# Optimization experiments

Hardware: AMD Instinct MI355X
Metric: run time of the kernel (lower is better)

Reference implementation:

```python
import jax, jax.numpy as jnp
import numpy as np

K = 100000      # tag vocab size
D_CLIP = 512    # Chinese-CLIP text dim
D_HID = 1024    # ProjectionHead hidden
D_OUT = 256     # proj_dim
B, P = 1024, 50
EPS = 1e-12


def setup_inputs() -> dict:
    key = jax.random.key(0)
    k_tab, k_ids, k_w1, k_b1, k_w2, k_b2 = jax.random.split(key, 6)
    # Frozen, L2-normalised base embeddings [K, 512]
    tab = jax.random.normal(k_tab, (K, D_CLIP), dtype=jnp.float32)
    tab = tab / jnp.maximum(jnp.linalg.norm(tab, axis=-1, keepdims=True), EPS)
    # tag ids in [-1, K): -1 marks padding rows
    tag_ids = jax.random.randint(k_ids, (B, P), -1, K, dtype=jnp.int64)
    # ProjectionHead params: Linear(512,1024) -> GELU -> Linear(1024,256)
    w1 = jax.random.normal(k_w1, (D_CLIP, D_HID), dtype=jnp.float32) * (1.0 / np.sqrt(D_CLIP))
    b1 = jnp.zeros((D_HID,), dtype=jnp.float32)
    w2 = jax.random.normal(k_w2, (D_HID, D_OUT), dtype=jnp.float32) * (1.0 / np.sqrt(D_HID))
    b2 = jnp.zeros((D_OUT,), dtype=jnp.float32)
    return {"tag_base_embs": tab, "w1": w1, "b1": b1, "w2": w2, "b2": b2,
            "tag_ids": tag_ids}


def reference(tag_base_embs, w1, b1, w2, b2, tag_ids):
    pad_mask = tag_ids < 0                       # [B, P]
    clamped = jnp.maximum(tag_ids, 0)
    flat = tag_base_embs[clamped.reshape(-1)]    # [B*P, 512] gather
    h = jax.nn.gelu(flat @ w1 + b1)              # [B*P, 1024]
    y = h @ w2 + b2                              # [B*P, 256]
    y = y / jnp.maximum(jnp.linalg.norm(y, axis=-1, keepdims=True), EPS)
    y = y.reshape(tag_ids.shape[0], tag_ids.shape[1], -1)  # [B, P, 256]
    return jnp.where(pad_mask[..., None], 0.0, y)
```

## Files before the change

kernel.cpp:

```cpp
#include <hip/hip_runtime.h>
#include <hip/hip_bf16.h>
#include <cstdint>


typedef __bf16 bf16;
typedef bf16  bf16x8 __attribute__((ext_vector_type(8)));
typedef bf16  bf16x4 __attribute__((ext_vector_type(4)));
typedef float f32x4  __attribute__((ext_vector_type(4)));

#define D_IN    512
#define D_HID   1024
#define D_OUT   256
#define MT      64
#define CHUNK   256
#define NCH     4
#define NKS1    16
#define NKS2C   8
#define THREADS 512

#define OFF_A    0
#define OFF_H    65536
#define OFF_NS   (65536 + 65536)
#define OFF_RID  (65536 + 65536 + 2048)
#define LDS_TOTAL (65536 + 65536 + 2048 + 256)

#define W1F_ELEMS (64 * 16 * 64 * 8)

__device__ __forceinline__ float gelu_tanh(float x) {
  float u = 0.7978845608028654f * (x + 0.044715f * x * x * x);
  return x * __builtin_amdgcn_rcpf(1.0f + __expf(-2.0f * u));
}

__global__ void prep_weights(const float* __restrict__ w1, const float* __restrict__ w2,
                             bf16* __restrict__ w1f, bf16* __restrict__ w2f) {
  const int t = blockIdx.x * blockDim.x + threadIdx.x;
  if (t < 65536) {
    const int l  = t & 63;
    const int ks = (t >> 6) & 15;
    const int ct = t >> 10;
    const int col   = ct * 16 + (l & 15);
    const int kbase = ks * 32 + (l >> 4) * 8;
    bf16x8 o;
#pragma unroll
    for (int j = 0; j < 8; ++j) o[j] = (bf16)w1[(size_t)(kbase + j) * D_HID + col];
    *(bf16x8*)(w1f + (size_t)t * 8) = o;
  } else if (t < 65536 + 32768) {
    const int t2 = t - 65536;
    const int l   = t2 & 63;
    const int ks2 = (t2 >> 6) & 31;
    const int ct2 = t2 >> 11;
    const int col   = ct2 * 16 + (l & 15);
    const int kbase = ks2 * 32 + (l >> 4) * 8;
    bf16x8 o;
#pragma unroll
    for (int j = 0; j < 8; ++j) o[j] = (bf16)w2[(size_t)(kbase + j) * D_OUT + col];
    *(bf16x8*)(w2f + (size_t)t2 * 8) = o;
  }
}

__global__ __launch_bounds__(THREADS, 2)
void tagproj_fused(const float* __restrict__ tab, const int* __restrict__ ids,
                   const bf16* __restrict__ w1f, const bf16* __restrict__ w2f,
                   const float* __restrict__ b1, const float* __restrict__ b2,
                   float* __restrict__ out) {
  extern __shared__ __align__(16) char lds[];
  bf16*  As  = (bf16*)(lds + OFF_A);
  bf16*  Hb  = (bf16*)(lds + OFF_H);
  float* Ns  = (float*)(lds + OFF_NS);
  int*   Rid = (int*)(lds + OFF_RID);

  const int tid = threadIdx.x;
  const int w   = tid >> 6;
  const int l   = tid & 63;
  const int lg  = l >> 4;
  const int lc  = l & 15;
  const int m0  = blockIdx.x * MT;

  {
    const int row = tid >> 3;
    const int q   = tid & 7;
    const int id  = ids[m0 + row];
    if (q == 0) Rid[row] = id;
    const float* src = tab + (size_t)(id < 0 ? 0 : id) * D_IN;
#pragma unroll
    for (int i = 0; i < 16; ++i) {
      const int c4 = i * 32 + q * 4;
      const float4 v = *(const float4*)(src + c4);
      bf16x4 b;
      b[0] = (bf16)v.x; b[1] = (bf16)v.y; b[2] = (bf16)v.z; b[3] = (bf16)v.w;
      *(bf16x4*)&As[row * 512 + (c4 ^ ((row & 15) << 3))] = b;
    }
  }
  __syncthreads();

  f32x4 acc2[4][2];
#pragma unroll
  for (int rt = 0; rt < 4; ++rt)
#pragma unroll
    for (int t = 0; t < 2; ++t) acc2[rt][t] = (f32x4){0.f, 0.f, 0.f, 0.f};

  for (int c = 0; c < NCH; ++c) {
    bf16* Hs = Hb + (c & 1) * (MT * CHUNK);

    f32x4 acc1[4][2];
#pragma unroll
    for (int rt = 0; rt < 4; ++rt)
#pragma unroll
      for (int t = 0; t < 2; ++t) acc1[rt][t] = (f32x4){0.f, 0.f, 0.f, 0.f};

    const bf16* w1p = w1f + (((size_t)(c * 16 + w * 2) * 16) * 64 + l) * 8;

    bf16x8 wr1[4][2];
#pragma unroll
    for (int pf = 0; pf < 2; ++pf)
#pragma unroll
      for (int t = 0; t < 2; ++t)
        wr1[pf][t] = *(const bf16x8*)(w1p + (size_t)t * 8192 + (size_t)pf * 512);

#pragma unroll
    for (int ks = 0; ks < NKS1; ++ks) {
      if (ks + 2 < NKS1) {
#pragma unroll
        for (int t = 0; t < 2; ++t)
          wr1[(ks + 2) & 3][t] =
              *(const bf16x8*)(w1p + (size_t)t * 8192 + (size_t)(ks + 2) * 512);
      }
      bf16x8 af[4];
#pragma unroll
      for (int rt = 0; rt < 4; ++rt) {
        const int e = ks * 32 + lg * 8;
        af[rt] = *(const bf16x8*)&As[(rt * 16 + lc) * 512 + (e ^ (lc << 3))];
      }
#pragma unroll
      for (int t = 0; t < 2; ++t)
#pragma unroll
        for (int rt = 0; rt < 4; ++rt)
          acc1[rt][t] = __builtin_amdgcn_mfma_f32_16x16x32_bf16(
              af[rt], wr1[ks & 3][t], acc1[rt][t], 0, 0, 0);
    }

#pragma unroll
    for (int t = 0; t < 2; ++t) {
      const int pos    = w * 2 + t;
      const float bias = b1[c * CHUNK + pos * 16 + lc];
#pragma unroll
      for (int rt = 0; rt < 4; ++rt) {
#pragma unroll
        for (int r = 0; r < 4; ++r) {
          const float x  = acc1[rt][t][r] + bias;
          const float hx = gelu_tanh(x);
          const int row  = rt * 16 + lg * 4 + r;
          const int e    = pos * 16 + lc;
          Hs[row * 256 + (e ^ ((row & 15) << 3))] = (bf16)hx;
        }
      }
    }
    __syncthreads();

    const bf16* w2p = w2f + (((size_t)(w * 2) * 32 + c * 8) * 64 + l) * 8;

    bf16x8 wr2[4][2];
#pragma unroll
    for (int pf = 0; pf < 2; ++pf)
#pragma unroll
      for (int t = 0; t < 2; ++t)
        wr2[pf][t] = *(const bf16x8*)(w2p + (size_t)t * 16384 + (size_t)pf * 512);

#pragma unroll
    for (int s2 = 0; s2 < NKS2C; ++s2) {
      if (s2 + 2 < NKS2C) {
#pragma unroll
        for (int t = 0; t < 2; ++t)
          wr2[(s2 + 2) & 3][t] =
              *(const bf16x8*)(w2p + (size_t)t * 16384 + (size_t)(s2 + 2) * 512);
      }
      bf16x8 hf[4];
#pragma unroll
      for (int rt = 0; rt < 4; ++rt) {
        const int e = s2 * 32 + lg * 8;
        hf[rt] = *(const bf16x8*)&Hs[(rt * 16 + lc) * 256 + (e ^ (lc << 3))];
      }
#pragma unroll
      for (int t = 0; t < 2; ++t)
#pragma unroll
        for (int rt = 0; rt < 4; ++rt)
          acc2[rt][t] = __builtin_amdgcn_mfma_f32_16x16x32_bf16(
              hf[rt], wr2[s2 & 3][t], acc2[rt][t], 0, 0, 0);
    }
  }

  float yv[4][2][4];
  float ssq[4][4];
#pragma unroll
  for (int rt = 0; rt < 4; ++rt)
#pragma unroll
    for (int r = 0; r < 4; ++r) ssq[rt][r] = 0.f;

#pragma unroll
  for (int t = 0; t < 2; ++t) {
    const float bias = b2[(w * 2 + t) * 16 + lc];
#pragma unroll
    for (int rt = 0; rt < 4; ++rt)
#pragma unroll
      for (int r = 0; r < 4; ++r) {
        const float v = acc2[rt][t][r] + bias;
        yv[rt][t][r] = v;
        ssq[rt][r] += v * v;
      }
  }
#pragma unroll
  for (int rt = 0; rt < 4; ++rt)
#pragma unroll
    for (int r = 0; r < 4; ++r) {
      float s = ssq[rt][r];
      s += __shfl_xor(s, 1);
      s += __shfl_xor(s, 2);
      s += __shfl_xor(s, 4);
      s += __shfl_xor(s, 8);
      ssq[rt][r] = s;
    }
  if (lc == 0) {
#pragma unroll
    for (int rt = 0; rt < 4; ++rt)
#pragma unroll
      for (int r = 0; r < 4; ++r)
        Ns[(rt * 16 + lg * 4 + r) * 8 + w] = ssq[rt][r];
  }
  __syncthreads();

#pragma unroll
  for (int rt = 0; rt < 4; ++rt)
#pragma unroll
    for (int r = 0; r < 4; ++r) {
      const int row = rt * 16 + lg * 4 + r;
      float ss = 0.f;
#pragma unroll
      for (int ww = 0; ww < 8; ++ww) ss += Ns[row * 8 + ww];
      const float scale = (Rid[row] < 0) ? 0.f : (1.f / fmaxf(sqrtf(ss), 1e-12f));
#pragma unroll
      for (int t = 0; t < 2; ++t)
        out[(size_t)(m0 + row) * D_OUT + (w * 2 + t) * 16 + lc] = yv[rt][t][r] * scale;
    }
}

extern "C" void kernel_launch(void* const* d_in, const int* in_sizes, int n_in,
                              void* d_out, int out_size, void* d_ws, size_t ws_size,
                              hipStream_t stream) {
  const float* tab = (const float*)d_in[0];
  const float* w1  = (const float*)d_in[1];
  const float* b1  = (const float*)d_in[2];
  const float* w2  = (const float*)d_in[3];
  const float* b2  = (const float*)d_in[4];
  const int*   ids = (const int*)d_in[5];
  float* out = (float*)d_out;

  bf16* w1f = (bf16*)d_ws;
  bf16* w2f = w1f + W1F_ELEMS;

  hipLaunchKernelGGL(prep_weights, dim3(384), dim3(256), 0, stream, w1, w2, w1f, w2f);

  (void)hipFuncSetAttribute(reinterpret_cast<const void*>(tagproj_fused),
                            hipFuncAttributeMaxDynamicSharedMemorySize, LDS_TOTAL);
  hipLaunchKernelGGL(tagproj_fused, dim3(51200 / MT), dim3(THREADS), LDS_TOTAL, stream,
                     tab, ids, w1f, w2f, b1, b2, out);
}
```

Before: 183.3 us.

## Rebalance rows per block with 32-row tiles and exact single-wave grid

Each block now owns 100 consecutive rows, processed as three 32-row tiles plus a 4-row tail tile. The launch is 512 blocks. Halving the tile size halves LDS use, so two blocks can be resident per CU and the whole grid fits in one wave. This removes the partial final wave of the old 800-block, 64-row launch. In exchange each weight fragment loaded from L2 feeds half as many MFMA rows, which doubles weight traffic, and the tail tile wastes MFMA work on padded rows.

```diff
diff --git a/kernel.cpp b/kernel.cpp
--- a/kernel.cpp
+++ b/kernel.cpp
@@ -11,18 +11,20 @@
 #define D_IN    512
 #define D_HID   1024
 #define D_OUT   256
-#define MT      64
+#define MT      32
+#define RPB     100
 #define CHUNK   256
 #define NCH     4
 #define NKS1    16
 #define NKS2C   8
 #define THREADS 512
+#define NROWS   51200
 
 #define OFF_A    0
-#define OFF_H    65536
-#define OFF_NS   (65536 + 65536)
-#define OFF_RID  (65536 + 65536 + 2048)
-#define LDS_TOTAL (65536 + 65536 + 2048 + 256)
+#define OFF_H    32768
+#define OFF_NS   (32768 + 32768)
+#define OFF_RID  (32768 + 32768 + 1024)
+#define LDS_TOTAL (32768 + 32768 + 1024 + 128)
 
 #define W1F_ELEMS (64 * 16 * 64 * 8)
 
@@ -58,7 +60,187 @@
   }
 }
 
-__global__ __launch_bounds__(THREADS, 2)
+template<int RT, int RV>
+__device__ __forceinline__ void process_tile(
+    const float* __restrict__ tab, const int* __restrict__ ids,
+    const bf16* __restrict__ w1f, const bf16* __restrict__ w2f,
+    const float* __restrict__ b1, const float* __restrict__ b2,
+    float* __restrict__ out,
+    bf16* As, bf16* Hb, float* Ns, int* Rid,
+    int row0, int tid, int w, int l, int lg, int lc) {
+
+  __syncthreads();
+
+  {
+    const int row = tid >> 4;
+    const int q   = tid & 15;
+    int id = -1;
+    if (RV == MT || row < RV) id = ids[row0 + row];
+    if (q == 0) Rid[row] = id;
+    const float* src = tab + (size_t)(id < 0 ? 0 : id) * D_IN;
+#pragma unroll
+    for (int i = 0; i < 8; ++i) {
+      const int c4 = i * 64 + q * 4;
+      const float4 v = *(const float4*)(src + c4);
+      bf16x4 b;
+      b[0] = (bf16)v.x; b[1] = (bf16)v.y; b[2] = (bf16)v.z; b[3] = (bf16)v.w;
+      *(bf16x4*)&As[row * 512 + (c4 ^ ((row & 15) << 3))] = b;
+    }
+  }
+  __syncthreads();
+
+  f32x4 acc2[RT][2];
+#pragma unroll
+  for (int rt = 0; rt < RT; ++rt)
+#pragma unroll
+    for (int t = 0; t < 2; ++t) acc2[rt][t] = (f32x4){0.f, 0.f, 0.f, 0.f};
+
+  for (int c = 0; c < NCH; ++c) {
+    bf16* Hs = Hb + (c & 1) * (MT * CHUNK);
+
+    f32x4 acc1[RT][2];
+#pragma unroll
+    for (int rt = 0; rt < RT; ++rt)
+#pragma unroll
+      for (int t = 0; t < 2; ++t) acc1[rt][t] = (f32x4){0.f, 0.f, 0.f, 0.f};
+
+    const bf16* w1p = w1f + (((size_t)(c * 16 + w * 2) * 16) * 64 + l) * 8;
+    bf16x8 wr1[4][2];
+#pragma unroll
+    for (int pf = 0; pf < 2; ++pf)
+#pragma unroll
+      for (int t = 0; t < 2; ++t)
+        wr1[pf][t] = *(const bf16x8*)(w1p + (size_t)t * 8192 + (size_t)pf * 512);
+
+#pragma unroll
+    for (int ks = 0; ks < NKS1; ++ks) {
+      if (ks + 2 < NKS1) {
+#pragma unroll
+        for (int t = 0; t < 2; ++t)
+          wr1[(ks + 2) & 3][t] =
+              *(const bf16x8*)(w1p + (size_t)t * 8192 + (size_t)(ks + 2) * 512);
+      }
+      bf16x8 af[RT];
+#pragma unroll
+      for (int rt = 0; rt < RT; ++rt) {
+        const int e = ks * 32 + lg * 8;
+        af[rt] = *(const bf16x8*)&As[(rt * 16 + lc) * 512 + (e ^ (lc << 3))];
+      }
+#pragma unroll
+      for (int t = 0; t < 2; ++t)
+#pragma unroll
+        for (int rt = 0; rt < RT; ++rt)
+          acc1[rt][t] = __builtin_amdgcn_mfma_f32_16x16x32_bf16(
+              af[rt], wr1[ks & 3][t], acc1[rt][t], 0, 0, 0);
+    }
+
+#pragma unroll
+    for (int t = 0; t < 2; ++t) {
+      const int pos    = w * 2 + t;
+      const float bias = b1[c * CHUNK + pos * 16 + lc];
+#pragma unroll
+      for (int rt = 0; rt < RT; ++rt) {
+#pragma unroll
+        for (int r = 0; r < 4; ++r) {
+          const float x  = acc1[rt][t][r] + bias;
+          const float hx = gelu_tanh(x);
+          const int row  = rt * 16 + lg * 4 + r;
+          const int e    = pos * 16 + lc;
+          Hs[row * 256 + (e ^ ((row & 15) << 3))] = (bf16)hx;
+        }
+      }
+    }
+    __syncthreads();
+
+    const bf16* w2p = w2f + (((size_t)(w * 2) * 32 + c * 8) * 64 + l) * 8;
+    bf16x8 wr2[4][2];
+#pragma unroll
+    for (int pf = 0; pf < 2; ++pf)
+#pragma unroll
+      for (int t = 0; t < 2; ++t)
+        wr2[pf][t] = *(const bf16x8*)(w2p + (size_t)t * 16384 + (size_t)pf * 512);
+
+#pragma unroll
+    for (int s2 = 0; s2 < NKS2C; ++s2) {
+      if (s2 + 2 < NKS2C) {
+#pragma unroll
+        for (int t = 0; t < 2; ++t)
+          wr2[(s2 + 2) & 3][t] =
+              *(const bf16x8*)(w2p + (size_t)t * 16384 + (size_t)(s2 + 2) * 512);
+      }
+      bf16x8 hf[RT];
+#pragma unroll
+      for (int rt = 0; rt < RT; ++rt) {
+        const int e = s2 * 32 + lg * 8;
+        hf[rt] = *(const bf16x8*)&Hs[(rt * 16 + lc) * 256 + (e ^ (lc << 3))];
+      }
+#pragma unroll
+      for (int t = 0; t < 2; ++t)
+#pragma unroll
+        for (int rt = 0; rt < RT; ++rt)
+          acc2[rt][t] = __builtin_amdgcn_mfma_f32_16x16x32_bf16(
+              hf[rt], wr2[s2 & 3][t], acc2[rt][t], 0, 0, 0);
+    }
+  }
+
+  float yv[RT][2][4];
+  float ssq[RT][4];
+#pragma unroll
+  for (int rt = 0; rt < RT; ++rt)
+#pragma unroll
+    for (int r = 0; r < 4; ++r) ssq[rt][r] = 0.f;
+
+#pragma unroll
+  for (int t = 0; t < 2; ++t) {
+    const float bias = b2[(w * 2 + t) * 16 + lc];
+#pragma unroll
+    for (int rt = 0; rt < RT; ++rt)
+#pragma unroll
+      for (int r = 0; r < 4; ++r) {
+        const float v = acc2[rt][t][r] + bias;
+        yv[rt][t][r] = v;
+        ssq[rt][r] += v * v;
+      }
+  }
+#pragma unroll
+  for (int rt = 0; rt < RT; ++rt)
+#pragma unroll
+    for (int r = 0; r < 4; ++r) {
+      float s = ssq[rt][r];
+      s += __shfl_xor(s, 1);
+      s += __shfl_xor(s, 2);
+      s += __shfl_xor(s, 4);
+      s += __shfl_xor(s, 8);
+      ssq[rt][r] = s;
+    }
+  if (lc == 0) {
+#pragma unroll
+    for (int rt = 0; rt < RT; ++rt)
+#pragma unroll
+      for (int r = 0; r < 4; ++r)
+        Ns[(rt * 16 + lg * 4 + r) * 8 + w] = ssq[rt][r];
+  }
+  __syncthreads();
+
+#pragma unroll
+  for (int rt = 0; rt < RT; ++rt)
+#pragma unroll
+    for (int r = 0; r < 4; ++r) {
+      const int row = rt * 16 + lg * 4 + r;
+      if (RV == MT || row < RV) {
+        float ss = 0.f;
+#pragma unroll
+        for (int ww = 0; ww < 8; ++ww) ss += Ns[row * 8 + ww];
+        const float scale = (Rid[row] < 0) ? 0.f : (1.f / fmaxf(sqrtf(ss), 1e-12f));
+#pragma unroll
+        for (int t = 0; t < 2; ++t)
+          out[(size_t)(row0 + row) * D_OUT + w * 32 + t * 16 + lc] =
+              yv[rt][t][r] * scale;
+      }
+    }
+}
+
+__global__ __launch_bounds__(THREADS, 4)
 void tagproj_fused(const float* __restrict__ tab, const int* __restrict__ ids,
                    const bf16* __restrict__ w1f, const bf16* __restrict__ w2f,
                    const float* __restrict__ b1, const float* __restrict__ b2,
@@ -74,173 +256,13 @@
   const int l   = tid & 63;
   const int lg  = l >> 4;
   const int lc  = l & 15;
-  const int m0  = blockIdx.x * MT;
-
-  {
-    const int row = tid >> 3;
-    const int q   = tid & 7;
-    const int id  = ids[m0 + row];
-    if (q == 0) Rid[row] = id;
-    const float* src = tab + (size_t)(id < 0 ? 0 : id) * D_IN;
-#pragma unroll
-    for (int i = 0; i < 16; ++i) {
-      const int c4 = i * 32 + q * 4;
-      const float4 v = *(const float4*)(src + c4);
-      bf16x4 b;
-      b[0] = (bf16)v.x; b[1] = (bf16)v.y; b[2] = (bf16)v.z; b[3] = (bf16)v.w;
-      *(bf16x4*)&As[row * 512 + (c4 ^ ((row & 15) << 3))] = b;
-    }
-  }
-  __syncthreads();
-
-  f32x4 acc2[4][2];
-#pragma unroll
-  for (int rt = 0; rt < 4; ++rt)
-#pragma unroll
-    for (int t = 0; t < 2; ++t) acc2[rt][t] = (f32x4){0.f, 0.f, 0.f, 0.f};
-
-  for (int c = 0; c < NCH; ++c) {
-    bf16* Hs = Hb + (c & 1) * (MT * CHUNK);
-
-    f32x4 acc1[4][2];
-#pragma unroll
-    for (int rt = 0; rt < 4; ++rt)
-#pragma unroll
-      for (int t = 0; t < 2; ++t) acc1[rt][t] = (f32x4){0.f, 0.f, 0.f, 0.f};
-
-    const bf16* w1p = w1f + (((size_t)(c * 16 + w * 2) * 16) * 64 + l) * 8;
-
-    bf16x8 wr1[4][2];
-#pragma unroll
-    for (int pf = 0; pf < 2; ++pf)
-#pragma unroll
-      for (int t = 0; t < 2; ++t)
-        wr1[pf][t] = *(const bf16x8*)(w1p + (size_t)t * 8192 + (size_t)pf * 512);
-
-#pragma unroll
-    for (int ks = 0; ks < NKS1; ++ks) {
-      if (ks + 2 < NKS1) {
-#pragma unroll
-        for (int t = 0; t < 2; ++t)
-          wr1[(ks + 2) & 3][t] =
-              *(const bf16x8*)(w1p + (size_t)t * 8192 + (size_t)(ks + 2) * 512);
-      }
-      bf16x8 af[4];
-#pragma unroll
-      for (int rt = 0; rt < 4; ++rt) {
-        const int e = ks * 32 + lg * 8;
-        af[rt] = *(const bf16x8*)&As[(rt * 16 + lc) * 512 + (e ^ (lc << 3))];
-      }
-#pragma unroll
-      for (int t = 0; t < 2; ++t)
-#pragma unroll
-        for (int rt = 0; rt < 4; ++rt)
-          acc1[rt][t] = __builtin_amdgcn_mfma_f32_16x16x32_bf16(
-              af[rt], wr1[ks & 3][t], acc1[rt][t], 0, 0, 0);
-    }
-
-#pragma unroll
-    for (int t = 0; t < 2; ++t) {
-      const int pos    = w * 2 + t;
-      const float bias = b1[c * CHUNK + pos * 16 + lc];
-#pragma unroll
-      for (int rt = 0; rt < 4; ++rt) {
-#pragma unroll
-        for (int r = 0; r < 4; ++r) {
-          const float x  = acc1[rt][t][r] + bias;
-          const float hx = gelu_tanh(x);
-          const int row  = rt * 16 + lg * 4 + r;
-          const int e    = pos * 16 + lc;
-          Hs[row * 256 + (e ^ ((row & 15) << 3))] = (bf16)hx;
-        }
-      }
-    }
-    __syncthreads();
-
-    const bf16* w2p = w2f + (((size_t)(w * 2) * 32 + c * 8) * 64 + l) * 8;
-
-    bf16x8 wr2[4][2];
-#pragma unroll
-    for (int pf = 0; pf < 2; ++pf)
-#pragma unroll
-      for (int t = 0; t < 2; ++t)
-        wr2[pf][t] = *(const bf16x8*)(w2p + (size_t)t * 16384 + (size_t)pf * 512);
-
-#pragma unroll
-    for (int s2 = 0; s2 < NKS2C; ++s2) {
-      if (s2 + 2 < NKS2C) {
-#pragma unroll
-        for (int t = 0; t < 2; ++t)
-          wr2[(s2 + 2) & 3][t] =
-              *(const bf16x8*)(w2p + (size_t)t * 16384 + (size_t)(s2 + 2) * 512);
-      }
-      bf16x8 hf[4];
-#pragma unroll
-      for (int rt = 0; rt < 4; ++rt) {
-        const int e = s2 * 32 + lg * 8;
-        hf[rt] = *(const bf16x8*)&Hs[(rt * 16 + lc) * 256 + (e ^ (lc << 3))];
-      }
-#pragma unroll
-      for (int t = 0; t < 2; ++t)
-#pragma unroll
-        for (int rt = 0; rt < 4; ++rt)
-          acc2[rt][t] = __builtin_amdgcn_mfma_f32_16x16x32_bf16(
-              hf[rt], wr2[s2 & 3][t], acc2[rt][t], 0, 0, 0);
-    }
-  }
-
-  float yv[4][2][4];
-  float ssq[4][4];
-#pragma unroll
-  for (int rt = 0; rt < 4; ++rt)
-#pragma unroll
-    for (int r = 0; r < 4; ++r) ssq[rt][r] = 0.f;
-
-#pragma unroll
-  for (int t = 0; t < 2; ++t) {
-    const float bias = b2[(w * 2 + t) * 16 + lc];
-#pragma unroll
-    for (int rt = 0; rt < 4; ++rt)
-#pragma unroll
-      for (int r = 0; r < 4; ++r) {
-        const float v = acc2[rt][t][r] + bias;
-        yv[rt][t][r] = v;
-        ssq[rt][r] += v * v;
-      }
-  }
-#pragma unroll
-  for (int rt = 0; rt < 4; ++rt)
-#pragma unroll
-    for (int r = 0; r < 4; ++r) {
-      float s = ssq[rt][r];
-      s += __shfl_xor(s, 1);
-      s += __shfl_xor(s, 2);
-      s += __shfl_xor(s, 4);
-      s += __shfl_xor(s, 8);
-      ssq[rt][r] = s;
-    }
-  if (lc == 0) {
-#pragma unroll
-    for (int rt = 0; rt < 4; ++rt)
-#pragma unroll
-      for (int r = 0; r < 4; ++r)
-        Ns[(rt * 16 + lg * 4 + r) * 8 + w] = ssq[rt][r];
-  }
-  __syncthreads();
-
-#pragma unroll
-  for (int rt = 0; rt < 4; ++rt)
-#pragma unroll
-    for (int r = 0; r < 4; ++r) {
-      const int row = rt * 16 + lg * 4 + r;
-      float ss = 0.f;
-#pragma unroll
-      for (int ww = 0; ww < 8; ++ww) ss += Ns[row * 8 + ww];
-      const float scale = (Rid[row] < 0) ? 0.f : (1.f / fmaxf(sqrtf(ss), 1e-12f));
-#pragma unroll
-      for (int t = 0; t < 2; ++t)
-        out[(size_t)(m0 + row) * D_OUT + (w * 2 + t) * 16 + lc] = yv[rt][t][r] * scale;
-    }
+  const int base = blockIdx.x * RPB;
+
+  for (int tt = 0; tt < 3; ++tt)
+    process_tile<2, MT>(tab, ids, w1f, w2f, b1, b2, out,
+                        As, Hb, Ns, Rid, base + tt * MT, tid, w, l, lg, lc);
+  process_tile<1, 4>(tab, ids, w1f, w2f, b1, b2, out,
+                     As, Hb, Ns, Rid, base + 96, tid, w, l, lg, lc);
 }
 
 extern "C" void kernel_launch(void* const* d_in, const int* in_sizes, int n_in,
@@ -261,6 +283,6 @@
 
   (void)hipFuncSetAttribute(reinterpret_cast<const void*>(tagproj_fused),
                             hipFuncAttributeMaxDynamicSharedMemorySize, LDS_TOTAL);
-  hipLaunchKernelGGL(tagproj_fused, dim3(51200 / MT), dim3(THREADS), LDS_TOTAL, stream,
+  hipLaunchKernelGGL(tagproj_fused, dim3(NROWS / RPB), dim3(THREADS), LDS_TOTAL, stream,
                      tab, ids, w1f, w2f, b1, b2, out);
 }
```

Result: slower. 247.7 us (+35.1%).
